# Optimization experiments

Hardware: AMD Instinct MI355X
Metric: run time of the kernel (lower is better)

## Reference

```python
import jax, jax.numpy as jnp
import numpy as np

B, IN, OUT = 65536, 1024, 1024
NB, D, H, L = 16, 32, 64, 4      # n_bundles, bundle_dim, norm_mlp hidden, n_latent_layers
TOT = NB * D                      # total latent dim = 512 (also encoder/decoder hidden)


def setup_inputs() -> dict:
    key = jax.random.key(0)
    ks = jax.random.split(key, 20)
    rn = lambda k, shape, s=0.02: (jax.random.normal(k, shape, dtype=jnp.float32) * s)
    return {
        "x": jax.random.normal(ks[0], (B, IN), dtype=jnp.float32),
        # encoder: Linear(IN,TOT), Linear(TOT,TOT), Linear(TOT,TOT)
        "enc_w1": rn(ks[1], (TOT, IN)), "enc_b1": jnp.zeros((TOT,), jnp.float32),
        "enc_w2": rn(ks[2], (TOT, TOT)), "enc_b2": jnp.zeros((TOT,), jnp.float32),
        "enc_w3": rn(ks[3], (TOT, TOT)), "enc_b3": jnp.zeros((TOT,), jnp.float32),
        # per-latent-layer norm_mlp: Linear(NB,H)+b, Linear(H,H)+b, Linear(H,NB) no bias
        "mlp1_w": rn(ks[4], (L, H, NB)), "mlp1_b": jnp.zeros((L, H), jnp.float32),
        "mlp2_w": rn(ks[5], (L, H, H)),  "mlp2_b": jnp.zeros((L, H), jnp.float32),
        "mlp3_w": rn(ks[6], (L, NB, H)),
        # mixing_weights[i][j] has shape (d_i, d_j); homogeneous -> [L,NB,NB,D,D], init 0.01*randn
        "mix_w": rn(ks[7], (L, NB, NB, D, D), 0.01),
        "gate_bias": jnp.zeros((L, NB), jnp.float32),
        # decoder: Linear(TOT,TOT), Linear(TOT,TOT), Linear(TOT,OUT)
        "dec_w1": rn(ks[8], (TOT, TOT)), "dec_b1": jnp.zeros((TOT,), jnp.float32),
        "dec_w2": rn(ks[9], (TOT, TOT)), "dec_b2": jnp.zeros((TOT,), jnp.float32),
        "dec_w3": rn(ks[10], (OUT, TOT)), "dec_b3": jnp.zeros((OUT,), jnp.float32),
    }


def _gelu(v):
    return jax.nn.gelu(v, approximate=False)  # torch nn.GELU default (erf)


def _soft_equivariant(z, m1w, m1b, m2w, m2b, m3w, mw, gb):
    # z: [B, TOT] -> bundles [B, NB, D] (homogeneous dims, contiguous split == reshape)
    zb = z.reshape(z.shape[0], NB, D)
    norms = jnp.linalg.norm(zb, axis=-1) + 1e-8          # [B, NB]
    h = _gelu(norms @ m1w.T + m1b)                        # [B, H]
    h = _gelu(h @ m2w.T + m2b)                            # [B, H]
    scales = jax.nn.softplus(h @ m3w.T)                   # [B, NB]
    equi = zb * scales[:, :, None]                        # [B, NB, D]
    # mixed_i = sum_j F.linear(bundles[j], W[i][j]) = bundles[j] @ W[i][j].T
    mixed = jnp.einsum('bjd,ijed->bie', zb, mw)           # [B, NB, D]
    gates = jax.nn.sigmoid(gb)                            # [NB]
    combined = equi + gates[None, :, None] * mixed        # [B, NB, D]
    return z + combined.reshape(z.shape[0], TOT)          # residual


def reference(x, enc_w1, enc_b1, enc_w2, enc_b2, enc_w3, enc_b3,
              mlp1_w, mlp1_b, mlp2_w, mlp2_b, mlp3_w, mix_w, gate_bias,
              dec_w1, dec_b1, dec_w2, dec_b2, dec_w3, dec_b3):
    # encoder
    z = _gelu(x @ enc_w1.T + enc_b1)
    z = _gelu(z @ enc_w2.T + enc_b2)
    z = z @ enc_w3.T + enc_b3
    # latent dynamics: L SoftEquivariantLayers (fixed small loop over layers)
    for l in range(L):
        z = _soft_equivariant(z, mlp1_w[l], mlp1_b[l], mlp2_w[l], mlp2_b[l],
                              mlp3_w[l], mix_w[l], gate_bias[l])
    # decoder
    y = _gelu(z @ dec_w1.T + dec_b1)
    y = _gelu(y @ dec_w2.T + dec_b2)
    return y @ dec_w3.T + dec_b3
```

## Files before the change

### kernel.cpp

```cpp
#include <hip/hip_runtime.h>
#include <hip/hip_bf16.h>

typedef float f32x4 __attribute__((ext_vector_type(4)));
typedef __bf16 bf16x8 __attribute__((ext_vector_type(8)));
typedef unsigned short u16x8 __attribute__((ext_vector_type(8)));
typedef unsigned short u16;

__device__ __forceinline__ u16 f2bf(float f) {
  __bf16 h = (__bf16)f;
  return __builtin_bit_cast(u16, h);
}
__device__ __forceinline__ float bf2f(u16 s) {
  return __uint_as_float(((unsigned int)s) << 16);
}
__device__ __forceinline__ float gelu_f(float x) {
  return 0.5f * x * (1.0f + erff(x * 0.70710678118654752f));
}
__device__ __forceinline__ void gload_lds16(const void* g, void* l) {
  __builtin_amdgcn_global_load_lds((const __attribute__((address_space(1))) void*)g,
                                   (__attribute__((address_space(3))) void*)l, 16, 0, 0);
}
#define MFMA(a, b, c) __builtin_amdgcn_mfma_f32_16x16x32_bf16((a), (b), (c), 0, 0, 0)
#define BARRIER_PINNED() do { \
    __builtin_amdgcn_s_barrier(); \
    asm volatile("" ::: "memory"); \
    __builtin_amdgcn_sched_barrier(0); \
  } while (0)

__global__ void cvt_all(const float* __restrict__ e1, const float* __restrict__ e2,
                        const float* __restrict__ e3, const float* __restrict__ d1,
                        const float* __restrict__ d2, const float* __restrict__ d3,
                        const float* __restrict__ mx, u16* __restrict__ dst)
{
  int i = blockIdx.x * blockDim.x + threadIdx.x;
  int stride = gridDim.x * blockDim.x;
  for (; i < 3145728; i += stride) {
    float v;
    if (i < 524288)        v = e1[i];
    else if (i < 786432)   v = e2[i - 524288];
    else if (i < 1048576)  v = e3[i - 786432];
    else if (i < 1310720)  v = d1[i - 1048576];
    else if (i < 1572864)  v = d2[i - 1310720];
    else if (i < 2097152)  v = d3[i - 1572864];
    else {
      int j = i - 2097152;
      int l = j >> 18, rem = j & 262143;
      int o = rem >> 9, k = rem & 511;
      int bi = o >> 5, e = o & 31, jj = k >> 5, dd = k & 31;
      v = mx[(((l * 16 + bi) * 16 + jj) * 32 + e) * 32 + dd];
    }
    dst[i] = f2bf(v);
  }
}

__global__ void cvt_x(const float* __restrict__ s, u16* __restrict__ d) {
  int i = blockIdx.x * blockDim.x + threadIdx.x;
  int stride = gridDim.x * blockDim.x;
  for (; i < 8388608; i += stride) {
    float4 v0 = *(const float4*)(s + (size_t)i * 8);
    float4 v1 = *(const float4*)(s + (size_t)i * 8 + 4);
    u16x8 u;
    u[0] = f2bf(v0.x); u[1] = f2bf(v0.y); u[2] = f2bf(v0.z); u[3] = f2bf(v0.w);
    u[4] = f2bf(v1.x); u[5] = f2bf(v1.y); u[6] = f2bf(v1.z); u[7] = f2bf(v1.w);
    *(u16x8*)(d + (size_t)i * 8) = u;
  }
}

__device__ __forceinline__ void stage_AB(const u16* __restrict__ Ab,
                                         const u16* __restrict__ Bb, int K,
                                         u16* At, u16* Bt, int wid, int lane)
{
  #pragma unroll
  for (int it = 0; it < 4; ++it) {
    int c = ((it * 4 + wid) << 6) + lane;
    int row = c >> 3;
    int cb = (c & 7) << 4;
    const char* g = (const char*)(Ab + (size_t)row * K) + (cb ^ ((row & 7) << 4));
    gload_lds16(g, (char*)At + ((it * 4 + wid) << 10));
  }
  #pragma unroll
  for (int it = 0; it < 2; ++it) {
    int c = ((it * 4 + wid) << 6) + lane;
    int row = c >> 3;
    int cb = (c & 7) << 4;
    const char* g = (const char*)(Bb + (size_t)row * K) + (cb ^ ((row & 7) << 4));
    gload_lds16(g, (char*)Bt + ((it * 4 + wid) << 10));
  }
}

template<int EPI>
__global__ __launch_bounds__(256, 2)
void gemm_p(const u16* __restrict__ A, const u16* __restrict__ Bw,
            const float* __restrict__ bias, void* __restrict__ Cp,
            const u16* __restrict__ zOld, const float* __restrict__ scales,
            const float* __restrict__ gateBias, int M, int N, int K)
{
  __shared__ u16 At[3][128 * 64];
  __shared__ u16 Bt[3][64 * 64];
  const int tid = threadIdx.x;
  const int lane = tid & 63;
  const int wid = tid >> 6;

  const int nx = N >> 6;
  const int ny = M >> 7;
  const int d = blockIdx.x;
  const int xcd = d & 7;
  const int seq = d >> 3;
  const int by = xcd * (ny >> 3) + seq / nx;
  const int bx = seq - (seq / nx) * nx;
  const int m0 = by << 7;
  const int n0 = bx << 6;

  const int wr = wid >> 1, wc = wid & 1;
  const int r16 = lane & 15;
  const int kg = (lane >> 4) << 3;
  const int sw = (r16 & 7) << 4;

  const u16* Ab = A + (size_t)m0 * K;
  const u16* Bb = Bw + (size_t)n0 * K;
  const int NT = K >> 6;

  f32x4 acc[4][2] = {};

  stage_AB(Ab,      Bb,      K, At[0], Bt[0], wid, lane);
  stage_AB(Ab + 64, Bb + 64, K, At[1], Bt[1], wid, lane);

  int cb = 0, ib = 2;
  for (int kt = 0; kt < NT; ++kt) {
    if (kt + 1 < NT) { asm volatile("s_waitcnt vmcnt(6)" ::: "memory"); }
    else             { asm volatile("s_waitcnt vmcnt(0)" ::: "memory"); }
    BARRIER_PINNED();

    if (kt + 2 < NT) {
      stage_AB(Ab + ((kt + 2) << 6), Bb + ((kt + 2) << 6), K, At[ib], Bt[ib], wid, lane);
      ib = (ib == 2) ? 0 : ib + 1;
    }

    const char* Ac = (const char*)At[cb];
    const char* Bc = (const char*)Bt[cb];
    #pragma unroll
    for (int kk = 0; kk < 64; kk += 32) {
      const int kb = ((kk + kg) << 1) ^ sw;
      bf16x8 av[4], bv[2];
      #pragma unroll
      for (int m = 0; m < 4; ++m)
        av[m] = *(const bf16x8*)(Ac + (wr * 64 + m * 16 + r16) * 128 + kb);
      #pragma unroll
      for (int n = 0; n < 2; ++n)
        bv[n] = *(const bf16x8*)(Bc + (wc * 32 + n * 16 + r16) * 128 + kb);
      __builtin_amdgcn_s_setprio(1);
      #pragma unroll
      for (int m = 0; m < 4; ++m)
        #pragma unroll
        for (int n = 0; n < 2; ++n)
          acc[m][n] = MFMA(av[m], bv[n], acc[m][n]);
      __builtin_amdgcn_s_setprio(0);
    }
    cb = (cb == 2) ? 0 : cb + 1;
  }

  const int colBase = n0 + wc * 32 + r16;
  const int rowBase = m0 + wr * 64 + ((lane >> 4) << 2);
  #pragma unroll
  for (int n = 0; n < 2; ++n) {
    int col = colBase + n * 16;
    float bv_ = 0.f, gate = 0.f;
    if constexpr (EPI == 0 || EPI == 1 || EPI == 3) bv_ = bias[col];
    if constexpr (EPI == 2) gate = 1.f / (1.f + expf(-gateBias[col >> 5]));
    #pragma unroll
    for (int m = 0; m < 4; ++m) {
      #pragma unroll
      for (int r = 0; r < 4; ++r) {
        int row = rowBase + m * 16 + r;
        float v = acc[m][n][r];
        if constexpr (EPI == 0) {
          ((u16*)Cp)[(size_t)row * N + col] = f2bf(gelu_f(v + bv_));
        } else if constexpr (EPI == 1) {
          ((u16*)Cp)[(size_t)row * N + col] = f2bf(v + bv_);
        } else if constexpr (EPI == 2) {
          float sc = scales[(size_t)row * 16 + (col >> 5)];
          float zo = bf2f(zOld[(size_t)row * 512 + col]);
          ((u16*)Cp)[(size_t)row * N + col] = f2bf(zo * (1.f + sc) + gate * v);
        } else {
          ((float*)Cp)[(size_t)row * N + col] = v + bv_;
        }
      }
    }
  }
}

__global__ __launch_bounds__(256, 2)
void gemm_enc1_legacy(const float* __restrict__ Af, const u16* __restrict__ Bw,
                      const float* __restrict__ bias, u16* __restrict__ Cp,
                      int M, int N, int K)
{
  __shared__ u16 At[2][128 * 64];
  __shared__ u16 Bt[2][64 * 64];
  const int tid = threadIdx.x;
  const int lane = tid & 63;
  const int wid = tid >> 6;
  const int nx = N >> 6;
  const int ny = M >> 7;
  const int d = blockIdx.x;
  const int xcd = d & 7;
  const int seq = d >> 3;
  const int by = xcd * (ny >> 3) + seq / nx;
  const int bx = seq - (seq / nx) * nx;
  const int m0 = by << 7;
  const int n0 = bx << 6;
  const int wr = wid >> 1, wc = wid & 1;
  const int r16 = lane & 15;
  const int kg = (lane >> 4) << 3;
  const int sw = (r16 & 7) << 4;
  const int NT = K >> 6;
  f32x4 acc[4][2] = {};
  float4 aA[8];

  #pragma unroll
  for (int it = 0; it < 4; ++it) {
    int c = it * 256 + tid;
    int row = c >> 3;
    int cbyte = (c & 7) << 4;
    const float* src = Af + (size_t)(m0 + row) * K + ((c & 7) << 3);
    float4 v0 = *(const float4*)src;
    float4 v1 = *(const float4*)(src + 4);
    u16x8 u;
    u[0] = f2bf(v0.x); u[1] = f2bf(v0.y); u[2] = f2bf(v0.z); u[3] = f2bf(v0.w);
    u[4] = f2bf(v1.x); u[5] = f2bf(v1.y); u[6] = f2bf(v1.z); u[7] = f2bf(v1.w);
    *(u16x8*)((char*)At[0] + row * 128 + (cbyte ^ ((row & 7) << 4))) = u;
  }
  #pragma unroll
  for (int it = 0; it < 2; ++it) {
    int c = ((it * 4 + wid) << 6) + lane;
    int row = c >> 3;
    int cbyte = (c & 7) << 4;
    const char* g = (const char*)(Bw + (size_t)(n0 + row) * K) + (cbyte ^ ((row & 7) << 4));
    gload_lds16(g, (char*)Bt[0] + ((it * 4 + wid) << 10));
  }
  __syncthreads();

  for (int kt = 0; kt < NT; ++kt) {
    const int cur = kt & 1;
    const bool hasNext = (kt + 1) < NT;
    if (hasNext) {
      const int kn = (kt + 1) << 6;
      #pragma unroll
      for (int it = 0; it < 4; ++it) {
        int c = it * 256 + tid;
        int row = c >> 3;
        const float* src = Af + (size_t)(m0 + row) * K + kn + ((c & 7) << 3);
        aA[it * 2]     = *(const float4*)src;
        aA[it * 2 + 1] = *(const float4*)(src + 4);
      }
      #pragma unroll
      for (int it = 0; it < 2; ++it) {
        int c = ((it * 4 + wid) << 6) + lane;
        int row = c >> 3;
        int cbyte = (c & 7) << 4;
        const char* g = (const char*)(Bw + (size_t)(n0 + row) * K + kn) + (cbyte ^ ((row & 7) << 4));
        gload_lds16(g, (char*)Bt[cur ^ 1] + ((it * 4 + wid) << 10));
      }
    }
    #pragma unroll
    for (int kk = 0; kk < 64; kk += 32) {
      const int kb = ((kk + kg) << 1) ^ sw;
      bf16x8 av[4], bv[2];
      #pragma unroll
      for (int m = 0; m < 4; ++m)
        av[m] = *(const bf16x8*)((const char*)At[cur] + (wr * 64 + m * 16 + r16) * 128 + kb);
      #pragma unroll
      for (int n = 0; n < 2; ++n)
        bv[n] = *(const bf16x8*)((const char*)Bt[cur] + (wc * 32 + n * 16 + r16) * 128 + kb);
      #pragma unroll
      for (int m = 0; m < 4; ++m)
        #pragma unroll
        for (int n = 0; n < 2; ++n)
          acc[m][n] = MFMA(av[m], bv[n], acc[m][n]);
    }
    if (hasNext) {
      #pragma unroll
      for (int it = 0; it < 4; ++it) {
        int c = it * 256 + tid;
        int row = c >> 3;
        int cbyte = (c & 7) << 4;
        float4 v0 = aA[it * 2], v1 = aA[it * 2 + 1];
        u16x8 u;
        u[0] = f2bf(v0.x); u[1] = f2bf(v0.y); u[2] = f2bf(v0.z); u[3] = f2bf(v0.w);
        u[4] = f2bf(v1.x); u[5] = f2bf(v1.y); u[6] = f2bf(v1.z); u[7] = f2bf(v1.w);
        *(u16x8*)((char*)At[cur ^ 1] + row * 128 + (cbyte ^ ((row & 7) << 4))) = u;
      }
    }
    __syncthreads();
  }

  const int colBase = n0 + wc * 32 + r16;
  const int rowBase = m0 + wr * 64 + ((lane >> 4) << 2);
  #pragma unroll
  for (int n = 0; n < 2; ++n) {
    int col = colBase + n * 16;
    float bv_ = bias[col];
    #pragma unroll
    for (int m = 0; m < 4; ++m)
      #pragma unroll
      for (int r = 0; r < 4; ++r) {
        int row = rowBase + m * 16 + r;
        Cp[(size_t)row * N + col] = f2bf(gelu_f(acc[m][n][r] + bv_));
      }
  }
}

__global__ __launch_bounds__(256, 2)
void norm_mlp2(const u16* __restrict__ z,
               const float* __restrict__ w1, const float* __restrict__ b1,
               const float* __restrict__ w2, const float* __restrict__ b2,
               const float* __restrict__ w3, float* __restrict__ scales)
{
  __shared__ float nrm[256][17];
  const int tid = threadIdx.x;
  const size_t base = (size_t)blockIdx.x << 8;

  #pragma unroll
  for (int p = 0; p < 16; ++p) {
    const int C = (p << 8) + tid;
    const int r = C >> 4, b = C & 15;
    const u16* zp = z + ((base + r) << 9) + (b << 5);
    float ss = 0.f;
    #pragma unroll
    for (int q = 0; q < 4; ++q) {
      u16x8 v = *(const u16x8*)(zp + q * 8);
      #pragma unroll
      for (int j = 0; j < 8; ++j) { float f = bf2f(v[j]); ss += f * f; }
    }
    nrm[r][b] = sqrtf(ss) + 1e-8f;
  }
  __syncthreads();

  float nr[16];
  #pragma unroll
  for (int i = 0; i < 16; ++i) nr[i] = nrm[tid][i];

  float h2[64];
  #pragma unroll
  for (int j = 0; j < 64; ++j) h2[j] = b2[j];

  for (int kt = 0; kt < 4; ++kt) {
    float h1t[16];
    #pragma unroll
    for (int k16 = 0; k16 < 16; ++k16) {
      const int k = (kt << 4) + k16;
      float t = b1[k];
      #pragma unroll
      for (int i = 0; i < 16; ++i) t += nr[i] * w1[k * 16 + i];
      h1t[k16] = gelu_f(t);
    }
    const float* w2t = w2 + (kt << 4);
    #pragma unroll
    for (int j = 0; j < 64; ++j) {
      float s = 0.f;
      #pragma unroll
      for (int k16 = 0; k16 < 16; ++k16) s += h1t[k16] * w2t[j * 64 + k16];
      h2[j] += s;
    }
  }
  #pragma unroll
  for (int j = 0; j < 64; ++j) h2[j] = gelu_f(h2[j]);

  float* srow = scales + ((base + tid) << 4);
  #pragma unroll
  for (int b = 0; b < 16; ++b) {
    float s = 0.f;
    #pragma unroll
    for (int k = 0; k < 64; ++k) s += h2[k] * w3[b * 64 + k];
    s = (s > 20.f) ? s : log1pf(expf(s));
    srow[b] = s;
  }
}

extern "C" void kernel_launch(void* const* d_in, const int* in_sizes, int n_in,
                              void* d_out, int out_size, void* d_ws, size_t ws_size,
                              hipStream_t stream)
{
  (void)in_sizes; (void)n_in; (void)out_size;
  const float* x      = (const float*)d_in[0];
  const float* enc_w1 = (const float*)d_in[1];
  const float* enc_b1 = (const float*)d_in[2];
  const float* enc_w2 = (const float*)d_in[3];
  const float* enc_b2 = (const float*)d_in[4];
  const float* enc_w3 = (const float*)d_in[5];
  const float* enc_b3 = (const float*)d_in[6];
  const float* mlp1_w = (const float*)d_in[7];
  const float* mlp1_b = (const float*)d_in[8];
  const float* mlp2_w = (const float*)d_in[9];
  const float* mlp2_b = (const float*)d_in[10];
  const float* mlp3_w = (const float*)d_in[11];
  const float* mix_w  = (const float*)d_in[12];
  const float* gate_b = (const float*)d_in[13];
  const float* dec_w1 = (const float*)d_in[14];
  const float* dec_b1 = (const float*)d_in[15];
  const float* dec_w2 = (const float*)d_in[16];
  const float* dec_b2 = (const float*)d_in[17];
  const float* dec_w3 = (const float*)d_in[18];
  const float* dec_b3 = (const float*)d_in[19];

  char* ws = (char*)d_ws;
  const int M = 65536;
  dim3 blk(256);
  const int g512  = 8  * 512;
  const int g1024 = 16 * 512;

  const bool bigWs = (ws_size >= 211812352ULL);
  u16 *xb, *zA, *zB;
  float* scales;
  u16* wBase;
  if (bigWs) {
    xb     = (u16*)ws;
    zA     = (u16*)(ws + 134217728ULL);
    zB     = (u16*)ws;
    scales = (float*)(ws + 201326592ULL);
    wBase  = (u16*)(ws + 205520896ULL);
  } else {
    xb     = nullptr;
    zA     = (u16*)ws;
    zB     = (u16*)(ws + 67108864ULL);
    scales = (float*)(ws + 134217728ULL);
    wBase  = (u16*)(ws + 138412032ULL);
  }
  u16* wE1 = wBase;
  u16* wE2 = wE1 + 524288;
  u16* wE3 = wE2 + 262144;
  u16* wD1 = wE3 + 262144;
  u16* wD2 = wD1 + 262144;
  u16* wD3 = wD2 + 262144;
  u16* wMix = wD3 + 524288;

  cvt_all<<<512, 256, 0, stream>>>(enc_w1, enc_w2, enc_w3, dec_w1, dec_w2, dec_w3,
                                   mix_w, wBase);

  if (bigWs) {
    cvt_x<<<2048, 256, 0, stream>>>(x, xb);
    gemm_p<0><<<g512, blk, 0, stream>>>(xb, wE1, enc_b1, zA, nullptr, nullptr, nullptr, M, 512, 1024);
  } else {
    gemm_enc1_legacy<<<g512, blk, 0, stream>>>(x, wE1, enc_b1, zA, M, 512, 1024);
  }
  gemm_p<0><<<g512, blk, 0, stream>>>(zA, wE2, enc_b2, zB, nullptr, nullptr, nullptr, M, 512, 512);
  gemm_p<1><<<g512, blk, 0, stream>>>(zB, wE3, enc_b3, zA, nullptr, nullptr, nullptr, M, 512, 512);

  u16* cur = zA;
  u16* nxt = zB;
  for (int l = 0; l < 4; ++l) {
    norm_mlp2<<<256, blk, 0, stream>>>(cur, mlp1_w + l * 1024, mlp1_b + l * 64,
                                       mlp2_w + l * 4096, mlp2_b + l * 64,
                                       mlp3_w + l * 1024, scales);
    gemm_p<2><<<g512, blk, 0, stream>>>(cur, wMix + (size_t)l * 262144, nullptr, nxt,
                                        cur, scales, gate_b + l * 16, M, 512, 512);
    u16* t = cur; cur = nxt; nxt = t;
  }

  gemm_p<0><<<g512, blk, 0, stream>>>(cur, wD1, dec_b1, nxt, nullptr, nullptr, nullptr, M, 512, 512);
  { u16* t = cur; cur = nxt; nxt = t; }
  gemm_p<0><<<g512, blk, 0, stream>>>(cur, wD2, dec_b2, nxt, nullptr, nullptr, nullptr, M, 512, 512);
  { u16* t = cur; cur = nxt; nxt = t; }
  gemm_p<3><<<g1024, blk, 0, stream>>>(cur, wD3, dec_b3, d_out, nullptr, nullptr, nullptr, M, 1024, 512);
}
```

Baseline: 1.408 ms.

## Use A-panel-resident GEMM kernel that sweeps all N tiles per row block

Adds a gemm_panel kernel that loads a full 128x512 bf16 A row-panel (128KB) into LDS once, then streams double-buffered B tiles across all output column tiles. This removes repeated A reloads across N tiles and lets the latent mixing epilogue read z_old from LDS instead of global memory. It is used for every K=512 GEMM, including the decoder's last layer with N=1024. It relies on 160KB dynamic LDS at 512 threads, so occupancy is lower, and the small-workspace fallback is dropped.

```diff
diff --git a/kernel.cpp b/kernel.cpp
--- a/kernel.cpp
+++ b/kernel.cpp
@@ -66,6 +66,130 @@
   }
 }
 
+template<int EPI>
+__global__ __launch_bounds__(512, 2)
+void gemm_panel(const u16* __restrict__ A, const u16* __restrict__ Bw,
+                const float* __restrict__ bias, void* __restrict__ Cp,
+                const float* __restrict__ scales, const float* __restrict__ gateBias,
+                int N)
+{
+  extern __shared__ char smem[];
+  char* Apan = smem;
+
+  const int tid = threadIdx.x;
+  const int lane = tid & 63;
+  const int wid = tid >> 6;
+  const int m0 = blockIdx.x << 7;
+
+  const int wr = wid >> 2;
+  const int wc = wid & 3;
+  const int r16 = lane & 15;
+  const int kg = (lane >> 4) << 3;
+  const int sw = (r16 & 7) << 4;
+
+  #pragma unroll
+  for (int it = 0; it < 16; ++it) {
+    int c = ((it * 8 + wid) << 6) + lane;
+    int row = c >> 6;
+    int cb = (c & 63) << 4;
+    const char* g = (const char*)(A + ((size_t)(m0 + row) << 9)) + (cb ^ ((row & 7) << 4));
+    gload_lds16(g, Apan + ((it * 8 + wid) << 10));
+  }
+  #pragma unroll
+  for (int it = 0; it < 2; ++it) {
+    int c = ((it * 8 + wid) << 6) + lane;
+    int row = c >> 3;
+    int cb = (c & 7) << 4;
+    const char* g = (const char*)(Bw + ((size_t)row << 9)) + (cb ^ ((row & 7) << 4));
+    gload_lds16(g, smem + 131072 + ((it * 8 + wid) << 10));
+  }
+
+  const int nN = N >> 7;
+  const int S = nN << 3;
+  f32x4 acc[4][2] = {};
+
+  for (int s = 0; s < S; ++s) {
+    const int kt = s & 7;
+    const int nt = s >> 3;
+
+    asm volatile("s_waitcnt vmcnt(0)" ::: "memory");
+    BARRIER_PINNED();
+
+    if (s + 1 < S) {
+      const int ktn = (s + 1) & 7;
+      const int ntn = (s + 1) >> 3;
+      char* dst = smem + 131072 + (((s + 1) & 1) << 14);
+      #pragma unroll
+      for (int it = 0; it < 2; ++it) {
+        int c = ((it * 8 + wid) << 6) + lane;
+        int row = c >> 3;
+        int cb = (c & 7) << 4;
+        const char* g = (const char*)(Bw + ((size_t)((ntn << 7) + row) << 9) + (ktn << 6))
+                        + (cb ^ ((row & 7) << 4));
+        gload_lds16(g, dst + ((it * 8 + wid) << 10));
+      }
+    }
+
+    const char* Bc = smem + 131072 + ((s & 1) << 14);
+    #pragma unroll
+    for (int kk = 0; kk < 64; kk += 32) {
+      const int kbA = ((kt << 7) + ((kk + kg) << 1)) ^ sw;
+      const int kbB = ((kk + kg) << 1) ^ sw;
+      bf16x8 av[4], bv[2];
+      #pragma unroll
+      for (int m = 0; m < 4; ++m)
+        av[m] = *(const bf16x8*)(Apan + ((wr * 64 + m * 16 + r16) << 10) + kbA);
+      #pragma unroll
+      for (int n = 0; n < 2; ++n)
+        bv[n] = *(const bf16x8*)(Bc + ((wc * 32 + n * 16 + r16) << 7) + kbB);
+      __builtin_amdgcn_s_setprio(1);
+      #pragma unroll
+      for (int m = 0; m < 4; ++m)
+        #pragma unroll
+        for (int n = 0; n < 2; ++n)
+          acc[m][n] = MFMA(av[m], bv[n], acc[m][n]);
+      __builtin_amdgcn_s_setprio(0);
+    }
+
+    if (kt == 7) {
+      const int colBase = (nt << 7) + wc * 32 + r16;
+      const int rowOff = wr * 64 + ((lane >> 4) << 2);
+      #pragma unroll
+      for (int n = 0; n < 2; ++n) {
+        const int col = colBase + n * 16;
+        float bv_ = 0.f, gate = 0.f;
+        if constexpr (EPI == 0 || EPI == 1 || EPI == 3) bv_ = bias[col];
+        if constexpr (EPI == 2) gate = 1.f / (1.f + expf(-gateBias[col >> 5]));
+        #pragma unroll
+        for (int m = 0; m < 4; ++m) {
+          #pragma unroll
+          for (int r = 0; r < 4; ++r) {
+            const int rloc = rowOff + m * 16 + r;
+            const int row = m0 + rloc;
+            float v = acc[m][n][r];
+            if constexpr (EPI == 0) {
+              ((u16*)Cp)[(size_t)row * N + col] = f2bf(gelu_f(v + bv_));
+            } else if constexpr (EPI == 1) {
+              ((u16*)Cp)[(size_t)row * N + col] = f2bf(v + bv_);
+            } else if constexpr (EPI == 2) {
+              float sc = scales[(size_t)row * 16 + (col >> 5)];
+              float zo = bf2f(*(const u16*)(Apan + ((size_t)rloc << 10) + (((col << 1)) ^ ((rloc & 7) << 4))));
+              ((u16*)Cp)[(size_t)row * N + col] = f2bf(zo * (1.f + sc) + gate * v);
+            } else {
+              ((float*)Cp)[(size_t)row * N + col] = v + bv_;
+            }
+          }
+        }
+      }
+      #pragma unroll
+      for (int m = 0; m < 4; ++m)
+        #pragma unroll
+        for (int n = 0; n < 2; ++n)
+          acc[m][n] = f32x4{0.f, 0.f, 0.f, 0.f};
+    }
+  }
+}
+
 __device__ __forceinline__ void stage_AB(const u16* __restrict__ Ab,
                                          const u16* __restrict__ Bb, int K,
                                          u16* At, u16* Bt, int wid, int lane)
@@ -88,12 +212,9 @@
   }
 }
 
-template<int EPI>
 __global__ __launch_bounds__(256, 2)
-void gemm_p(const u16* __restrict__ A, const u16* __restrict__ Bw,
-            const float* __restrict__ bias, void* __restrict__ Cp,
-            const u16* __restrict__ zOld, const float* __restrict__ scales,
-            const float* __restrict__ gateBias, int M, int N, int K)
+void gemm_p0(const u16* __restrict__ A, const u16* __restrict__ Bw,
+             const float* __restrict__ bias, u16* __restrict__ Cp, int M, int N, int K)
 {
   __shared__ u16 At[3][128 * 64];
   __shared__ u16 Bt[3][64 * 64];
@@ -164,140 +285,6 @@
   #pragma unroll
   for (int n = 0; n < 2; ++n) {
     int col = colBase + n * 16;
-    float bv_ = 0.f, gate = 0.f;
-    if constexpr (EPI == 0 || EPI == 1 || EPI == 3) bv_ = bias[col];
-    if constexpr (EPI == 2) gate = 1.f / (1.f + expf(-gateBias[col >> 5]));
-    #pragma unroll
-    for (int m = 0; m < 4; ++m) {
-      #pragma unroll
-      for (int r = 0; r < 4; ++r) {
-        int row = rowBase + m * 16 + r;
-        float v = acc[m][n][r];
-        if constexpr (EPI == 0) {
-          ((u16*)Cp)[(size_t)row * N + col] = f2bf(gelu_f(v + bv_));
-        } else if constexpr (EPI == 1) {
-          ((u16*)Cp)[(size_t)row * N + col] = f2bf(v + bv_);
-        } else if constexpr (EPI == 2) {
-          float sc = scales[(size_t)row * 16 + (col >> 5)];
-          float zo = bf2f(zOld[(size_t)row * 512 + col]);
-          ((u16*)Cp)[(size_t)row * N + col] = f2bf(zo * (1.f + sc) + gate * v);
-        } else {
-          ((float*)Cp)[(size_t)row * N + col] = v + bv_;
-        }
-      }
-    }
-  }
-}
-
-__global__ __launch_bounds__(256, 2)
-void gemm_enc1_legacy(const float* __restrict__ Af, const u16* __restrict__ Bw,
-                      const float* __restrict__ bias, u16* __restrict__ Cp,
-                      int M, int N, int K)
-{
-  __shared__ u16 At[2][128 * 64];
-  __shared__ u16 Bt[2][64 * 64];
-  const int tid = threadIdx.x;
-  const int lane = tid & 63;
-  const int wid = tid >> 6;
-  const int nx = N >> 6;
-  const int ny = M >> 7;
-  const int d = blockIdx.x;
-  const int xcd = d & 7;
-  const int seq = d >> 3;
-  const int by = xcd * (ny >> 3) + seq / nx;
-  const int bx = seq - (seq / nx) * nx;
-  const int m0 = by << 7;
-  const int n0 = bx << 6;
-  const int wr = wid >> 1, wc = wid & 1;
-  const int r16 = lane & 15;
-  const int kg = (lane >> 4) << 3;
-  const int sw = (r16 & 7) << 4;
-  const int NT = K >> 6;
-  f32x4 acc[4][2] = {};
-  float4 aA[8];
-
-  #pragma unroll
-  for (int it = 0; it < 4; ++it) {
-    int c = it * 256 + tid;
-    int row = c >> 3;
-    int cbyte = (c & 7) << 4;
-    const float* src = Af + (size_t)(m0 + row) * K + ((c & 7) << 3);
-    float4 v0 = *(const float4*)src;
-    float4 v1 = *(const float4*)(src + 4);
-    u16x8 u;
-    u[0] = f2bf(v0.x); u[1] = f2bf(v0.y); u[2] = f2bf(v0.z); u[3] = f2bf(v0.w);
-    u[4] = f2bf(v1.x); u[5] = f2bf(v1.y); u[6] = f2bf(v1.z); u[7] = f2bf(v1.w);
-    *(u16x8*)((char*)At[0] + row * 128 + (cbyte ^ ((row & 7) << 4))) = u;
-  }
-  #pragma unroll
-  for (int it = 0; it < 2; ++it) {
-    int c = ((it * 4 + wid) << 6) + lane;
-    int row = c >> 3;
-    int cbyte = (c & 7) << 4;
-    const char* g = (const char*)(Bw + (size_t)(n0 + row) * K) + (cbyte ^ ((row & 7) << 4));
-    gload_lds16(g, (char*)Bt[0] + ((it * 4 + wid) << 10));
-  }
-  __syncthreads();
-
-  for (int kt = 0; kt < NT; ++kt) {
-    const int cur = kt & 1;
-    const bool hasNext = (kt + 1) < NT;
-    if (hasNext) {
-      const int kn = (kt + 1) << 6;
-      #pragma unroll
-      for (int it = 0; it < 4; ++it) {
-        int c = it * 256 + tid;
-        int row = c >> 3;
-        const float* src = Af + (size_t)(m0 + row) * K + kn + ((c & 7) << 3);
-        aA[it * 2]     = *(const float4*)src;
-        aA[it * 2 + 1] = *(const float4*)(src + 4);
-      }
-      #pragma unroll
-      for (int it = 0; it < 2; ++it) {
-        int c = ((it * 4 + wid) << 6) + lane;
-        int row = c >> 3;
-        int cbyte = (c & 7) << 4;
-        const char* g = (const char*)(Bw + (size_t)(n0 + row) * K + kn) + (cbyte ^ ((row & 7) << 4));
-        gload_lds16(g, (char*)Bt[cur ^ 1] + ((it * 4 + wid) << 10));
-      }
-    }
-    #pragma unroll
-    for (int kk = 0; kk < 64; kk += 32) {
-      const int kb = ((kk + kg) << 1) ^ sw;
-      bf16x8 av[4], bv[2];
-      #pragma unroll
-      for (int m = 0; m < 4; ++m)
-        av[m] = *(const bf16x8*)((const char*)At[cur] + (wr * 64 + m * 16 + r16) * 128 + kb);
-      #pragma unroll
-      for (int n = 0; n < 2; ++n)
-        bv[n] = *(const bf16x8*)((const char*)Bt[cur] + (wc * 32 + n * 16 + r16) * 128 + kb);
-      #pragma unroll
-      for (int m = 0; m < 4; ++m)
-        #pragma unroll
-        for (int n = 0; n < 2; ++n)
-          acc[m][n] = MFMA(av[m], bv[n], acc[m][n]);
-    }
-    if (hasNext) {
-      #pragma unroll
-      for (int it = 0; it < 4; ++it) {
-        int c = it * 256 + tid;
-        int row = c >> 3;
-        int cbyte = (c & 7) << 4;
-        float4 v0 = aA[it * 2], v1 = aA[it * 2 + 1];
-        u16x8 u;
-        u[0] = f2bf(v0.x); u[1] = f2bf(v0.y); u[2] = f2bf(v0.z); u[3] = f2bf(v0.w);
-        u[4] = f2bf(v1.x); u[5] = f2bf(v1.y); u[6] = f2bf(v1.z); u[7] = f2bf(v1.w);
-        *(u16x8*)((char*)At[cur ^ 1] + row * 128 + (cbyte ^ ((row & 7) << 4))) = u;
-      }
-    }
-    __syncthreads();
-  }
-
-  const int colBase = n0 + wc * 32 + r16;
-  const int rowBase = m0 + wr * 64 + ((lane >> 4) << 2);
-  #pragma unroll
-  for (int n = 0; n < 2; ++n) {
-    int col = colBase + n * 16;
     float bv_ = bias[col];
     #pragma unroll
     for (int m = 0; m < 4; ++m)
@@ -376,11 +363,13 @@
   }
 }
 
+#define PANEL_SMEM 163840
+
 extern "C" void kernel_launch(void* const* d_in, const int* in_sizes, int n_in,
                               void* d_out, int out_size, void* d_ws, size_t ws_size,
                               hipStream_t stream)
 {
-  (void)in_sizes; (void)n_in; (void)out_size;
+  (void)in_sizes; (void)n_in; (void)out_size; (void)ws_size;
   const float* x      = (const float*)d_in[0];
   const float* enc_w1 = (const float*)d_in[1];
   const float* enc_b1 = (const float*)d_in[2];
@@ -404,27 +393,12 @@
 
   char* ws = (char*)d_ws;
   const int M = 65536;
-  dim3 blk(256);
-  const int g512  = 8  * 512;
-  const int g1024 = 16 * 512;
-
-  const bool bigWs = (ws_size >= 211812352ULL);
-  u16 *xb, *zA, *zB;
-  float* scales;
-  u16* wBase;
-  if (bigWs) {
-    xb     = (u16*)ws;
-    zA     = (u16*)(ws + 134217728ULL);
-    zB     = (u16*)ws;
-    scales = (float*)(ws + 201326592ULL);
-    wBase  = (u16*)(ws + 205520896ULL);
-  } else {
-    xb     = nullptr;
-    zA     = (u16*)ws;
-    zB     = (u16*)(ws + 67108864ULL);
-    scales = (float*)(ws + 134217728ULL);
-    wBase  = (u16*)(ws + 138412032ULL);
-  }
+
+  u16*   xb     = (u16*)ws;
+  u16*   zA     = (u16*)(ws + 134217728ULL);
+  u16*   zB     = (u16*)ws;
+  float* scales = (float*)(ws + 201326592ULL);
+  u16*   wBase  = (u16*)(ws + 205520896ULL);
   u16* wE1 = wBase;
   u16* wE2 = wE1 + 524288;
   u16* wE3 = wE2 + 262144;
@@ -433,32 +407,42 @@
   u16* wD3 = wD2 + 262144;
   u16* wMix = wD3 + 524288;
 
+  hipError_t e;
+  e = hipFuncSetAttribute(reinterpret_cast<const void*>(&gemm_panel<0>),
+                          hipFuncAttributeMaxDynamicSharedMemorySize, PANEL_SMEM);
+  e = hipFuncSetAttribute(reinterpret_cast<const void*>(&gemm_panel<1>),
+                          hipFuncAttributeMaxDynamicSharedMemorySize, PANEL_SMEM);
+  e = hipFuncSetAttribute(reinterpret_cast<const void*>(&gemm_panel<2>),
+                          hipFuncAttributeMaxDynamicSharedMemorySize, PANEL_SMEM);
+  e = hipFuncSetAttribute(reinterpret_cast<const void*>(&gemm_panel<3>),
+                          hipFuncAttributeMaxDynamicSharedMemorySize, PANEL_SMEM);
+  (void)e;
+
   cvt_all<<<512, 256, 0, stream>>>(enc_w1, enc_w2, enc_w3, dec_w1, dec_w2, dec_w3,
                                    mix_w, wBase);
 
-  if (bigWs) {
-    cvt_x<<<2048, 256, 0, stream>>>(x, xb);
-    gemm_p<0><<<g512, blk, 0, stream>>>(xb, wE1, enc_b1, zA, nullptr, nullptr, nullptr, M, 512, 1024);
-  } else {
-    gemm_enc1_legacy<<<g512, blk, 0, stream>>>(x, wE1, enc_b1, zA, M, 512, 1024);
-  }
-  gemm_p<0><<<g512, blk, 0, stream>>>(zA, wE2, enc_b2, zB, nullptr, nullptr, nullptr, M, 512, 512);
-  gemm_p<1><<<g512, blk, 0, stream>>>(zB, wE3, enc_b3, zA, nullptr, nullptr, nullptr, M, 512, 512);
+  dim3 pblk(512);
+  const int pgrid = 512;
+
+  cvt_x<<<2048, 256, 0, stream>>>(x, xb);
+  gemm_p0<<<8 * 512, dim3(256), 0, stream>>>(xb, wE1, enc_b1, zA, M, 512, 1024);
+  gemm_panel<0><<<pgrid, pblk, PANEL_SMEM, stream>>>(zA, wE2, enc_b2, zB, nullptr, nullptr, 512);
+  gemm_panel<1><<<pgrid, pblk, PANEL_SMEM, stream>>>(zB, wE3, enc_b3, zA, nullptr, nullptr, 512);
 
   u16* cur = zA;
   u16* nxt = zB;
   for (int l = 0; l < 4; ++l) {
-    norm_mlp2<<<256, blk, 0, stream>>>(cur, mlp1_w + l * 1024, mlp1_b + l * 64,
-                                       mlp2_w + l * 4096, mlp2_b + l * 64,
-                                       mlp3_w + l * 1024, scales);
-    gemm_p<2><<<g512, blk, 0, stream>>>(cur, wMix + (size_t)l * 262144, nullptr, nxt,
-                                        cur, scales, gate_b + l * 16, M, 512, 512);
+    norm_mlp2<<<256, dim3(256), 0, stream>>>(cur, mlp1_w + l * 1024, mlp1_b + l * 64,
+                                             mlp2_w + l * 4096, mlp2_b + l * 64,
+                                             mlp3_w + l * 1024, scales);
+    gemm_panel<2><<<pgrid, pblk, PANEL_SMEM, stream>>>(cur, wMix + (size_t)l * 262144,
+                                                       nullptr, nxt, scales, gate_b + l * 16, 512);
     u16* t = cur; cur = nxt; nxt = t;
   }
 
-  gemm_p<0><<<g512, blk, 0, stream>>>(cur, wD1, dec_b1, nxt, nullptr, nullptr, nullptr, M, 512, 512);
+  gemm_panel<0><<<pgrid, pblk, PANEL_SMEM, stream>>>(cur, wD1, dec_b1, nxt, nullptr, nullptr, 512);
   { u16* t = cur; cur = nxt; nxt = t; }
-  gemm_p<0><<<g512, blk, 0, stream>>>(cur, wD2, dec_b2, nxt, nullptr, nullptr, nullptr, M, 512, 512);
+  gemm_panel<0><<<pgrid, pblk, PANEL_SMEM, stream>>>(cur, wD2, dec_b2, nxt, nullptr, nullptr, 512);
   { u16* t = cur; cur = nxt; nxt = t; }
-  gemm_p<3><<<g1024, blk, 0, stream>>>(cur, wD3, dec_b3, d_out, nullptr, nullptr, nullptr, M, 1024, 512);
-}
+  gemm_panel<3><<<pgrid, pblk, PANEL_SMEM, stream>>>(cur, wD3, dec_b3, d_out, nullptr, nullptr, 1024);
+}
```

After: 1.388 ms. Within noise of the previous version (-1.4%).
